# Performance work log

Measured on AMD Instinct MI355X. Metric: run time of the kernel, lower is better.

## Reference

```python
import jax, jax.numpy as jnp
import numpy as np
from jax import lax

B, N, C = 4, 4096, 512
HEADS, SR = 8, 4
HW = 64  # spatial size, HW*HW == N
EPS = 1e-5


def setup_inputs() -> dict:
    key = jax.random.key(0)
    ks = jax.random.split(key, 12)
    s = 0.02
    return {
        "x": jax.random.normal(ks[0], (B, N, C), jnp.float32),
        "wq": jax.random.normal(ks[1], (C, C), jnp.float32) * s,
        "bq": jnp.zeros((C,), jnp.float32),
        "wk": jax.random.normal(ks[2], (C, C), jnp.float32) * s,
        "bk": jnp.zeros((C,), jnp.float32),
        "wv": jax.random.normal(ks[3], (C, C), jnp.float32) * s,
        "bv": jnp.zeros((C,), jnp.float32),
        "w_sr": jax.random.normal(ks[4], (SR, SR, C, C), jnp.float32) * s,  # HWIO
        "b_sr": jnp.zeros((C,), jnp.float32),
        "gamma": jnp.ones((C,), jnp.float32),
        "beta": jnp.zeros((C,), jnp.float32),
        "wp": jax.random.normal(ks[5], (C, C), jnp.float32) * s,
        "bp": jnp.zeros((C,), jnp.float32),
    }


def _layernorm(x, gamma, beta):
    mu = jnp.mean(x, axis=-1, keepdims=True)
    var = jnp.mean(jnp.square(x - mu), axis=-1, keepdims=True)
    return (x - mu) * lax.rsqrt(var + EPS) * gamma + beta


def reference(x, wq, bq, wk, bk, wv, bv, w_sr, b_sr, gamma, beta, wp, bp):
    b, n, c = x.shape
    dh = c // HEADS
    scale = dh ** (-0.5)
    # Q at full resolution: [b, heads, n, dh]
    q = (x @ wq + bq).reshape(b, n, HEADS, dh).transpose(0, 2, 1, 3)
    # spatial reduction of K/V: conv stride=kernel=SR (VALID)
    xr = x.reshape(b, HW, HW, c)
    xr = lax.conv_general_dilated(
        xr, w_sr, window_strides=(SR, SR), padding="VALID",
        dimension_numbers=("NHWC", "HWIO", "NHWC")) + b_sr
    xr = xr.reshape(b, -1, c)  # [b, n_kv, c]
    xr = _layernorm(xr, gamma, beta)
    n_kv = xr.shape[1]
    k = (xr @ wk + bk).reshape(b, n_kv, HEADS, dh).transpose(0, 2, 1, 3)
    v = (xr @ wv + bv).reshape(b, n_kv, HEADS, dh).transpose(0, 2, 1, 3)
    attn = jnp.einsum("bhqd,bhkd->bhqk", q, k) * scale
    attn = jax.nn.softmax(attn, axis=-1)
    out = jnp.einsum("bhqk,bhkd->bhqd", attn, v)
    out = out.transpose(0, 2, 1, 3).reshape(b, n, c)
    return out @ wp + bp
```

## Files before the change

### kernel.cpp

```cpp
#include <hip/hip_runtime.h>
#include <hip/hip_bf16.h>


#define EPSV 1e-5f
#define SCALE_Q 0.18033688011112042f

typedef __attribute__((ext_vector_type(8))) short short8v;
typedef __attribute__((ext_vector_type(4))) short short4v;
typedef __attribute__((ext_vector_type(4))) float float4v;

static __device__ __forceinline__ ushort f2bf_bits(float x) {
  __hip_bfloat16 h = __float2bfloat16(x);
  return *(ushort*)&h;
}

static __device__ __forceinline__ float4v mfma16(short8v a, short8v b, float4v c) {
  return __builtin_amdgcn_mfma_f32_16x16x32_bf16(a, b, c, 0, 0, 0);
}

static __device__ __forceinline__ void wr_chunk(ushort* lds, int base, int4 v) {
  *(int2*)&lds[base]       = make_int2(v.x, v.y);
  *(int2*)&lds[base + 128] = make_int2(v.z, v.w);
}

static __device__ __forceinline__ void tile_t32(const float* __restrict__ src, int srcld,
                                                ushort* __restrict__ dst, int dstld,
                                                int kr0, int c0, int tid, float (*t)[33]) {
  {
    const int r = tid >> 3, c4 = (tid & 7) * 4;
    const float4 v = *(const float4*)&src[(size_t)(kr0 + r) * srcld + c0 + c4];
    t[r][c4 + 0] = v.x; t[r][c4 + 1] = v.y; t[r][c4 + 2] = v.z; t[r][c4 + 3] = v.w;
  }
  __syncthreads();
  {
    const int n = tid >> 3, k4 = (tid & 7) * 4;
    short4v o;
#pragma unroll
    for (int i = 0; i < 4; ++i) o[i] = (short)f2bf_bits(t[k4 + i][n]);
    *(short4v*)&dst[(size_t)(c0 + n) * dstld + kr0 + k4] = o;
  }
}

__global__ __launch_bounds__(256)
void prep(const float* __restrict__ x, const float* __restrict__ wq,
          const float* __restrict__ wk, const float* __restrict__ wv,
          const float* __restrict__ wp, const float* __restrict__ wsr,
          const float* __restrict__ bk, const float* __restrict__ bv,
          ushort* __restrict__ xbf, ushort* __restrict__ wqT,
          ushort* __restrict__ wkvT, ushort* __restrict__ wpT,
          ushort* __restrict__ wsrT, float* __restrict__ bkv) {
  __shared__ float t[32][33];
  const int bid = blockIdx.x, tid = threadIdx.x;
  if (bid < 4096) {
    const int i = bid * 256 + tid;
    const float4* s4 = (const float4*)x;
    const float4 a = s4[2 * i], b = s4[2 * i + 1];
    short8v v;
    v[0] = (short)f2bf_bits(a.x); v[1] = (short)f2bf_bits(a.y);
    v[2] = (short)f2bf_bits(a.z); v[3] = (short)f2bf_bits(a.w);
    v[4] = (short)f2bf_bits(b.x); v[5] = (short)f2bf_bits(b.y);
    v[6] = (short)f2bf_bits(b.z); v[7] = (short)f2bf_bits(b.w);
    *(short8v*)&xbf[(size_t)i * 8] = v;
  } else if (bid < 8192) {
    const int tI = bid - 4096;
    const int kr0 = (tI & 255) * 32, c0 = (tI >> 8) * 32;
    tile_t32(wsr, 512, wsrT, 8192, kr0, c0, tid, t);
  } else if (bid < 9216) {
    const int wsel = (bid - 8192) >> 8;
    const int tI = (bid - 8192) & 255;
    const int kr0 = (tI & 15) * 32, c0 = (tI >> 4) * 32;
    const float* src = wsel == 0 ? wq : wsel == 1 ? wk : wsel == 2 ? wv : wp;
    ushort* dst = wsel == 0 ? wqT : wsel == 1 ? wkvT : wsel == 2 ? (wkvT + 262144) : wpT;
    tile_t32(src, 512, dst, 512, kr0, c0, tid, t);
  } else {
    const int i4 = tid * 4;
    const float4 v = (i4 < 512) ? *(const float4*)&bk[i4] : *(const float4*)&bv[i4 - 512];
    *(float4*)&bkv[i4] = v;
  }
}

template<int MODE>
__global__ __launch_bounds__(256)
void gemm_bf(const ushort* __restrict__ A, const ushort* __restrict__ BT,
             const float* __restrict__ bias, void* __restrict__ outp,
             int M, int N, int K, float scale) {
  __shared__ ushort lds[8192];
  const int tid = threadIdx.x;
  const int wave = tid >> 6, lane = tid & 63;
  const int wm = wave >> 1, wn = wave & 1;
  const int bm = blockIdx.x * 128, bn = blockIdx.y * 128;
  const int lid = lane & 15, lg = lane >> 4;
  const int r0 = tid >> 2, c8 = tid & 3;
  const int g0 = 2 * (c8 & 1), h2 = c8 >> 1;
  const int c0 = c8 * 8;
  const int basew = ((r0 >> 4) * 64 + 16 * g0 + (r0 & 15)) * 8 + h2 * 4;
  float4v acc[4][4];
  const float4v zf = {0.f, 0.f, 0.f, 0.f};
#pragma unroll
  for (int mi = 0; mi < 4; ++mi)
#pragma unroll
    for (int ni = 0; ni < 4; ++ni) acc[mi][ni] = zf;
  const ushort* Ar0 = A + (size_t)(bm + r0) * K;
  const ushort* Ar1 = Ar0 + (size_t)64 * K;
  const ushort* Br0 = BT + (size_t)(bn + r0) * K;
  const ushort* Br1 = Br0 + (size_t)64 * K;
  const int NK = K >> 5;
  int koff = c0;
  int4 pa0 = *(const int4*)(Ar0 + koff), pa1 = *(const int4*)(Ar1 + koff);
  int4 pb0 = *(const int4*)(Br0 + koff), pb1 = *(const int4*)(Br1 + koff);
  for (int kb = 0; kb < NK; ++kb) {
    wr_chunk(lds, basew, pa0);
    wr_chunk(lds, basew + 2048, pa1);
    wr_chunk(lds, basew + 4096, pb0);
    wr_chunk(lds, basew + 6144, pb1);
    __syncthreads();
    if (kb + 1 < NK) {
      koff += 32;
      pa0 = *(const int4*)(Ar0 + koff); pa1 = *(const int4*)(Ar1 + koff);
      pb0 = *(const int4*)(Br0 + koff); pb1 = *(const int4*)(Br1 + koff);
    }
    short8v af[4], bfr[4];
#pragma unroll
    for (int mi = 0; mi < 4; ++mi)
      af[mi] = *(const short8v*)&lds[((wm * 4 + mi) * 64 + lane) * 8];
#pragma unroll
    for (int ni = 0; ni < 4; ++ni)
      bfr[ni] = *(const short8v*)&lds[4096 + ((wn * 4 + ni) * 64 + lane) * 8];
#pragma unroll
    for (int mi = 0; mi < 4; ++mi)
#pragma unroll
      for (int ni = 0; ni < 4; ++ni) acc[mi][ni] = mfma16(af[mi], bfr[ni], acc[mi][ni]);
    __syncthreads();
  }
  float bvv[4];
#pragma unroll
  for (int ni = 0; ni < 4; ++ni) bvv[ni] = bias[bn + wn * 64 + ni * 16 + lid];
#pragma unroll
  for (int mi = 0; mi < 4; ++mi)
#pragma unroll
    for (int ni = 0; ni < 4; ++ni) {
      const int col = bn + wn * 64 + ni * 16 + lid;
#pragma unroll
      for (int reg = 0; reg < 4; ++reg) {
        const int row = bm + wm * 64 + mi * 16 + 4 * lg + reg;
        const float v = (acc[mi][ni][reg] + bvv[ni]) * scale;
        if (MODE == 0) ((float*)outp)[(size_t)row * N + col] = v;
        else if (MODE == 1) ((ushort*)outp)[(size_t)row * N + col] = f2bf_bits(v);
        else {
          if (col < 512) ((ushort*)outp)[(size_t)row * 512 + col] = f2bf_bits(v);
          else ((ushort*)outp)[524288 + (size_t)(col - 512) * 1024 + row] = f2bf_bits(v);
        }
      }
    }
}

static __device__ __forceinline__ int4 ld_patch(const ushort* xbf, int b, int oh, int ow, int kg) {
  const int ij = kg >> 9, ci = kg & 511;
  const int n = (oh * 4 + (ij >> 2)) * 64 + ow * 4 + (ij & 3);
  return *(const int4*)(xbf + ((size_t)b * 4096 + n) * 512 + ci);
}

__global__ __launch_bounds__(256)
void conv_bf(const ushort* __restrict__ xbf, const ushort* __restrict__ wsrT,
             float* __restrict__ part) {
  __shared__ ushort lds[8192];
  const int tid = threadIdx.x;
  const int wave = tid >> 6, lane = tid & 63;
  const int wm = wave >> 1, wn = wave & 1;
  const int bm = blockIdx.x * 128, bn = blockIdx.y * 128, z = blockIdx.z;
  const int lid = lane & 15, lg = lane >> 4;
  const int r0 = tid >> 2, c8 = tid & 3;
  const int g0 = 2 * (c8 & 1), h2 = c8 >> 1;
  const int c0 = c8 * 8;
  const int basew = ((r0 >> 4) * 64 + 16 * g0 + (r0 & 15)) * 8 + h2 * 4;
  const int p0 = bm + r0, p1 = p0 + 64;
  const int b0 = p0 >> 8, oh0 = (p0 & 255) >> 4, ow0 = p0 & 15;
  const int b1 = p1 >> 8, oh1 = (p1 & 255) >> 4, ow1 = p1 & 15;
  const ushort* Br0 = wsrT + (size_t)(bn + r0) * 8192;
  const ushort* Br1 = Br0 + (size_t)64 * 8192;
  float4v acc[4][4];
  const float4v zf = {0.f, 0.f, 0.f, 0.f};
#pragma unroll
  for (int mi = 0; mi < 4; ++mi)
#pragma unroll
    for (int ni = 0; ni < 4; ++ni) acc[mi][ni] = zf;
  int kg = z * 512 + c0;
  int4 pa0 = ld_patch(xbf, b0, oh0, ow0, kg);
  int4 pa1 = ld_patch(xbf, b1, oh1, ow1, kg);
  int4 pb0 = *(const int4*)(Br0 + kg);
  int4 pb1 = *(const int4*)(Br1 + kg);
  for (int kb = 0; kb < 16; ++kb) {
    wr_chunk(lds, basew, pa0);
    wr_chunk(lds, basew + 2048, pa1);
    wr_chunk(lds, basew + 4096, pb0);
    wr_chunk(lds, basew + 6144, pb1);
    __syncthreads();
    if (kb < 15) {
      kg += 32;
      pa0 = ld_patch(xbf, b0, oh0, ow0, kg);
      pa1 = ld_patch(xbf, b1, oh1, ow1, kg);
      pb0 = *(const int4*)(Br0 + kg);
      pb1 = *(const int4*)(Br1 + kg);
    }
    short8v af[4], bfr[4];
#pragma unroll
    for (int mi = 0; mi < 4; ++mi)
      af[mi] = *(const short8v*)&lds[((wm * 4 + mi) * 64 + lane) * 8];
#pragma unroll
    for (int ni = 0; ni < 4; ++ni)
      bfr[ni] = *(const short8v*)&lds[4096 + ((wn * 4 + ni) * 64 + lane) * 8];
#pragma unroll
    for (int mi = 0; mi < 4; ++mi)
#pragma unroll
      for (int ni = 0; ni < 4; ++ni) acc[mi][ni] = mfma16(af[mi], bfr[ni], acc[mi][ni]);
    __syncthreads();
  }
#pragma unroll
  for (int mi = 0; mi < 4; ++mi)
#pragma unroll
    for (int ni = 0; ni < 4; ++ni)
#pragma unroll
      for (int reg = 0; reg < 4; ++reg)
        part[(size_t)(z * 1024 + bm + wm * 64 + mi * 16 + 4 * lg + reg) * 512 +
             bn + wn * 64 + ni * 16 + lid] = acc[mi][ni][reg];
}

__global__ __launch_bounds__(256)
void reduce_ln(const float* __restrict__ part, const float* __restrict__ bsr,
               const float* __restrict__ gamma, const float* __restrict__ beta,
               ushort* __restrict__ xln) {
  const int wave = threadIdx.x >> 6;
  const int lane = threadIdx.x & 63;
  const int row = blockIdx.x * 4 + wave;
  const int c = lane * 8;
  float v[8];
  {
    const float4 a = *(const float4*)&bsr[c];
    const float4 b = *(const float4*)&bsr[c + 4];
    v[0] = a.x; v[1] = a.y; v[2] = a.z; v[3] = a.w;
    v[4] = b.x; v[5] = b.y; v[6] = b.z; v[7] = b.w;
  }
#pragma unroll
  for (int z = 0; z < 16; ++z) {
    const float* pr = &part[((size_t)z * 1024 + row) * 512 + c];
    const float4 a = *(const float4*)pr;
    const float4 b = *(const float4*)(pr + 4);
    v[0] += a.x; v[1] += a.y; v[2] += a.z; v[3] += a.w;
    v[4] += b.x; v[5] += b.y; v[6] += b.z; v[7] += b.w;
  }
  float sum = 0.f;
#pragma unroll
  for (int i = 0; i < 8; ++i) sum += v[i];
#pragma unroll
  for (int off = 32; off >= 1; off >>= 1) sum += __shfl_xor(sum, off);
  const float mu = sum * (1.0f / 512.0f);
  float sq = 0.f;
#pragma unroll
  for (int i = 0; i < 8; ++i) { v[i] -= mu; sq += v[i] * v[i]; }
#pragma unroll
  for (int off = 32; off >= 1; off >>= 1) sq += __shfl_xor(sq, off);
  const float rs = rsqrtf(sq * (1.0f / 512.0f) + EPSV);
  const float4 g1 = *(const float4*)&gamma[c];
  const float4 g2 = *(const float4*)&gamma[c + 4];
  const float4 e1 = *(const float4*)&beta[c];
  const float4 e2 = *(const float4*)&beta[c + 4];
  const float g[8] = {g1.x, g1.y, g1.z, g1.w, g2.x, g2.y, g2.z, g2.w};
  const float e[8] = {e1.x, e1.y, e1.z, e1.w, e2.x, e2.y, e2.z, e2.w};
  short8v ov;
#pragma unroll
  for (int i = 0; i < 8; ++i) ov[i] = (short)f2bf_bits(v[i] * rs * g[i] + e[i]);
  *(short8v*)&xln[(size_t)row * 512 + c] = ov;
}

__global__ __launch_bounds__(256)
void attn_bf(const ushort* __restrict__ qbf, const ushort* __restrict__ kbf,
             const ushort* __restrict__ vt, ushort* __restrict__ attno) {
  __shared__ ushort kv_lds[16384];
  const int bh = blockIdx.x, qt = blockIdx.y;
  const int b = bh >> 3, h = bh & 7;
  const int tid = threadIdx.x;
  const int wave = tid >> 6, lane = tid & 63;
  const int lid = lane & 15, lg = lane >> 4;
  {
    const ushort* Kb = kbf + (size_t)(b * 256) * 512 + h * 64;
#pragma unroll
    for (int i = 0; i < 8; ++i) {
      const int u = i * 256 + tid;
      const int kv = u >> 3, c8 = u & 7, d0 = c8 * 8;
      const int4 d = *(const int4*)(Kb + (size_t)kv * 512 + d0);
      const int f = (kv >> 4) * 2 + (d0 >> 5);
      const int g0 = (d0 >> 2) & 3, hh2 = (d0 >> 4) & 1;
      wr_chunk(kv_lds, (f * 64 + 16 * g0 + (kv & 15)) * 8 + hh2 * 4, d);
    }
  }
  short8v qfr[2][2];
  const int qrow0 = qt * 128 + wave * 32;
#pragma unroll
  for (int qf = 0; qf < 2; ++qf)
#pragma unroll
    for (int t = 0; t < 2; ++t) {
      const size_t base = (size_t)(b * 4096 + qrow0 + qf * 16 + lid) * 512 + h * 64 + 32 * t + 4 * lg;
      const short4v lo = *(const short4v*)&qbf[base];
      const short4v hi = *(const short4v*)&qbf[base + 16];
      short8v q;
      q[0] = lo[0]; q[1] = lo[1]; q[2] = lo[2]; q[3] = lo[3];
      q[4] = hi[0]; q[5] = hi[1]; q[6] = hi[2]; q[7] = hi[3];
      qfr[qf][t] = q;
    }
  __syncthreads();
  float4v s[16][2];
  const float4v zf = {0.f, 0.f, 0.f, 0.f};
#pragma unroll
  for (int kvf = 0; kvf < 16; ++kvf) { s[kvf][0] = zf; s[kvf][1] = zf; }
#pragma unroll
  for (int kvf = 0; kvf < 16; ++kvf)
#pragma unroll
    for (int t = 0; t < 2; ++t) {
      const short8v ka = *(const short8v*)&kv_lds[((kvf * 2 + t) * 64 + lane) * 8];
      s[kvf][0] = mfma16(ka, qfr[0][t], s[kvf][0]);
      s[kvf][1] = mfma16(ka, qfr[1][t], s[kvf][1]);
    }
  float inv[2];
#pragma unroll
  for (int qf = 0; qf < 2; ++qf) {
    float m = -1e30f;
#pragma unroll
    for (int kvf = 0; kvf < 16; ++kvf)
#pragma unroll
      for (int e = 0; e < 4; ++e) m = fmaxf(m, s[kvf][qf][e]);
    m = fmaxf(m, __shfl_xor(m, 16));
    m = fmaxf(m, __shfl_xor(m, 32));
    float sum = 0.f;
#pragma unroll
    for (int kvf = 0; kvf < 16; ++kvf)
#pragma unroll
      for (int e = 0; e < 4; ++e) {
        const float p = __builtin_amdgcn_exp2f(s[kvf][qf][e] - m);
        s[kvf][qf][e] = p;
        sum += p;
      }
    sum += __shfl_xor(sum, 16);
    sum += __shfl_xor(sum, 32);
    inv[qf] = 1.0f / sum;
  }
  __syncthreads();
  {
    const ushort* Vb = vt + (size_t)(h * 64) * 1024 + b * 256;
#pragma unroll
    for (int i = 0; i < 8; ++i) {
      const int u = i * 256 + tid;
      const int d = u >> 5, c8 = u & 31, kv0 = c8 * 8;
      const int4 dd = *(const int4*)(Vb + (size_t)d * 1024 + kv0);
      const int f = (d >> 4) * 8 + (kv0 >> 5);
      const int g0 = (kv0 >> 2) & 3, hh2 = (kv0 >> 4) & 1;
      wr_chunk(kv_lds, (f * 64 + 16 * g0 + (d & 15)) * 8 + hh2 * 4, dd);
    }
  }
  __syncthreads();
  float4v o[2][4];
#pragma unroll
  for (int qf = 0; qf < 2; ++qf)
#pragma unroll
    for (int nf = 0; nf < 4; ++nf) o[qf][nf] = zf;
#pragma unroll
  for (int t = 0; t < 8; ++t) {
    short8v vb[4];
#pragma unroll
    for (int nf = 0; nf < 4; ++nf)
      vb[nf] = *(const short8v*)&kv_lds[((nf * 8 + t) * 64 + lane) * 8];
#pragma unroll
    for (int qf = 0; qf < 2; ++qf) {
      short8v pa;
#pragma unroll
      for (int j = 0; j < 4; ++j) {
        pa[j]     = (short)f2bf_bits(s[2 * t][qf][j]);
        pa[4 + j] = (short)f2bf_bits(s[2 * t + 1][qf][j]);
      }
#pragma unroll
      for (int nf = 0; nf < 4; ++nf) o[qf][nf] = mfma16(pa, vb[nf], o[qf][nf]);
    }
  }
#pragma unroll
  for (int qf = 0; qf < 2; ++qf) {
    float sc[4];
#pragma unroll
    for (int reg = 0; reg < 4; ++reg) sc[reg] = __shfl(inv[qf], 4 * lg + reg);
#pragma unroll
    for (int nf = 0; nf < 4; ++nf)
#pragma unroll
      for (int reg = 0; reg < 4; ++reg) {
        const int q = qrow0 + qf * 16 + 4 * lg + reg;
        const int c = h * 64 + nf * 16 + lid;
        attno[(size_t)(b * 4096 + q) * 512 + c] = f2bf_bits(o[qf][nf][reg] * sc[reg]);
      }
  }
}

extern "C" void kernel_launch(void* const* d_in, const int* in_sizes, int n_in,
                              void* d_out, int out_size, void* d_ws, size_t ws_size,
                              hipStream_t stream) {
  const float* x     = (const float*)d_in[0];
  const float* wq    = (const float*)d_in[1];
  const float* bq    = (const float*)d_in[2];
  const float* wk    = (const float*)d_in[3];
  const float* bk    = (const float*)d_in[4];
  const float* wv    = (const float*)d_in[5];
  const float* bv    = (const float*)d_in[6];
  const float* wsr   = (const float*)d_in[7];
  const float* bsr   = (const float*)d_in[8];
  const float* gamma = (const float*)d_in[9];
  const float* beta  = (const float*)d_in[10];
  const float* wp    = (const float*)d_in[11];
  const float* bp    = (const float*)d_in[12];
  float* out = (float*)d_out;

  char* w = (char*)d_ws;
  ushort* xbf   = (ushort*)(w);
  ushort* qbf   = (ushort*)(w + 16777216);
  ushort* attno = (ushort*)(w + 33554432);
  float*  part  = (float*) (w + 50331648);
  ushort* wsrT  = (ushort*)(w + 83886080);
  ushort* wqT   = (ushort*)(w + 92274688);
  ushort* wpT   = (ushort*)(w + 92798976);
  ushort* wkvT  = (ushort*)(w + 93323264);
  ushort* xln   = (ushort*)(w + 94371840);
  ushort* kbf   = (ushort*)(w + 95420416);
  ushort* vt    = (ushort*)(w + 96468992);
  float*  bkv   = (float*) (w + 97517568);

  prep<<<9217, 256, 0, stream>>>(x, wq, wk, wv, wp, wsr, bk, bv,
                                 xbf, wqT, wkvT, wpT, wsrT, bkv);
  conv_bf<<<dim3(8, 4, 16), 256, 0, stream>>>(xbf, wsrT, part);
  reduce_ln<<<256, 256, 0, stream>>>(part, bsr, gamma, beta, xln);
  gemm_bf<2><<<dim3(8, 8), 256, 0, stream>>>(xln, wkvT, bkv, kbf, 1024, 1024, 512, 1.0f);
  gemm_bf<1><<<dim3(128, 4), 256, 0, stream>>>(xbf, wqT, bq, qbf, 16384, 512, 512, SCALE_Q);
  attn_bf<<<dim3(32, 32), 256, 0, stream>>>(qbf, kbf, vt, attno);
  gemm_bf<0><<<dim3(128, 4), 256, 0, stream>>>(attno, wpT, bp, out, 16384, 512, 512, 1.0f);
}
```

Before: 217.4 us.

## Fuse Q projection into attention kernel and pre-swizzle K/V into LDS image layout

The separate Q-projection GEMM is removed. Each attention block now computes its 128x64 Q tile directly from bf16 x and the transposed wq with MFMA, which avoids writing and re-reading the 16 MB qbf buffer and saves a launch. The KV GEMM epilogue writes K and V straight into the per-(batch,head) swizzled LDS layout, so the attention kernel loads them with plain contiguous int4 copies, and the V load is issued early to overlap with softmax. The cost is a redundant Q recomputation per head block (K=512 loop), more LDS per block, and scattered 2-byte stores in the KV GEMM epilogue.

Result: slower. 236.8 us (+8.9%).

```diff
diff --git a/kernel.cpp b/kernel.cpp
--- a/kernel.cpp
+++ b/kernel.cpp
@@ -144,11 +144,25 @@
       for (int reg = 0; reg < 4; ++reg) {
         const int row = bm + wm * 64 + mi * 16 + 4 * lg + reg;
         const float v = (acc[mi][ni][reg] + bvv[ni]) * scale;
-        if (MODE == 0) ((float*)outp)[(size_t)row * N + col] = v;
-        else if (MODE == 1) ((ushort*)outp)[(size_t)row * N + col] = f2bf_bits(v);
-        else {
-          if (col < 512) ((ushort*)outp)[(size_t)row * 512 + col] = f2bf_bits(v);
-          else ((ushort*)outp)[524288 + (size_t)(col - 512) * 1024 + row] = f2bf_bits(v);
+        if (MODE == 0) {
+          ((float*)outp)[(size_t)row * N + col] = v;
+        } else {
+          ushort* img = (ushort*)outp;
+          const int bb = row >> 8, kv = row & 255;
+          if (col < 512) {
+            const int hh = col >> 6, d = col & 63;
+            img[(size_t)(bb * 8 + hh) * 16384 +
+                ((kv >> 4) * 2 + (d >> 5)) * 512 +
+                ((kv & 15) + (((d >> 2) & 3) << 4)) * 8 +
+                (d & 3) + (((d >> 4) & 1) << 2)] = f2bf_bits(v);
+          } else {
+            const int c2 = col - 512;
+            const int hh = c2 >> 6, d = c2 & 63;
+            (img + 524288)[(size_t)(bb * 8 + hh) * 16384 +
+                ((d >> 4) * 8 + (kv >> 5)) * 512 +
+                ((d & 15) + (((kv >> 2) & 3) << 4)) * 8 +
+                (kv & 3) + (((kv >> 4) & 1) << 2)] = f2bf_bits(v);
+          }
         }
       }
     }
@@ -273,43 +287,77 @@
 }
 
 __global__ __launch_bounds__(256)
-void attn_bf(const ushort* __restrict__ qbf, const ushort* __restrict__ kbf,
-             const ushort* __restrict__ vt, ushort* __restrict__ attno) {
-  __shared__ ushort kv_lds[16384];
+void attn_fused(const ushort* __restrict__ xbf, const ushort* __restrict__ wqT,
+                const float* __restrict__ bq, const ushort* __restrict__ kvimg,
+                ushort* __restrict__ attno) {
+  __shared__ ushort kv_lds[22528];
   const int bh = blockIdx.x, qt = blockIdx.y;
   const int b = bh >> 3, h = bh & 7;
   const int tid = threadIdx.x;
   const int wave = tid >> 6, lane = tid & 63;
   const int lid = lane & 15, lg = lane >> 4;
-  {
-    const ushort* Kb = kbf + (size_t)(b * 256) * 512 + h * 64;
-#pragma unroll
-    for (int i = 0; i < 8; ++i) {
-      const int u = i * 256 + tid;
-      const int kv = u >> 3, c8 = u & 7, d0 = c8 * 8;
-      const int4 d = *(const int4*)(Kb + (size_t)kv * 512 + d0);
-      const int f = (kv >> 4) * 2 + (d0 >> 5);
-      const int g0 = (d0 >> 2) & 3, hh2 = (d0 >> 4) & 1;
-      wr_chunk(kv_lds, (f * 64 + 16 * g0 + (kv & 15)) * 8 + hh2 * 4, d);
-    }
+  const ushort* kimg = kvimg + (size_t)bh * 16384;
+  const ushort* vimg = kvimg + 524288 + (size_t)bh * 16384;
+  int4 kreg[8];
+#pragma unroll
+  for (int c = 0; c < 8; ++c)
+    kreg[c] = *(const int4*)(kimg + (c * 256 + tid) * 8);
+  const int r0 = tid >> 2, c8 = tid & 3;
+  const int g0 = 2 * (c8 & 1), h2 = c8 >> 1;
+  const int basew = ((r0 >> 4) * 64 + 16 * g0 + (r0 & 15)) * 8 + h2 * 4;
+  ushort* qs = kv_lds + 16384;
+  const ushort* Xr0 = xbf + (size_t)(b * 4096 + qt * 128 + r0) * 512;
+  const ushort* Xr1 = Xr0 + (size_t)64 * 512;
+  const ushort* Wr  = wqT + (size_t)(h * 64 + r0) * 512;
+  float4v accq[4][2];
+  const float4v zf = {0.f, 0.f, 0.f, 0.f};
+#pragma unroll
+  for (int dd = 0; dd < 4; ++dd) { accq[dd][0] = zf; accq[dd][1] = zf; }
+  int koff = c8 * 8;
+  int4 px0 = *(const int4*)(Xr0 + koff);
+  int4 px1 = *(const int4*)(Xr1 + koff);
+  int4 pw  = *(const int4*)(Wr + koff);
+  for (int kt = 0; kt < 16; ++kt) {
+    wr_chunk(qs, basew, px0);
+    wr_chunk(qs, basew + 2048, px1);
+    wr_chunk(qs, basew + 4096, pw);
+    __syncthreads();
+    if (kt < 15) {
+      koff += 32;
+      px0 = *(const int4*)(Xr0 + koff);
+      px1 = *(const int4*)(Xr1 + koff);
+      pw  = *(const int4*)(Wr + koff);
+    }
+    const short8v xf0 = *(const short8v*)&qs[((wave * 2 + 0) * 64 + lane) * 8];
+    const short8v xf1 = *(const short8v*)&qs[((wave * 2 + 1) * 64 + lane) * 8];
+#pragma unroll
+    for (int dd = 0; dd < 4; ++dd) {
+      const short8v wf = *(const short8v*)&qs[4096 + (dd * 64 + lane) * 8];
+      accq[dd][0] = mfma16(wf, xf0, accq[dd][0]);
+      accq[dd][1] = mfma16(wf, xf1, accq[dd][1]);
+    }
+    __syncthreads();
   }
   short8v qfr[2][2];
-  const int qrow0 = qt * 128 + wave * 32;
-#pragma unroll
-  for (int qf = 0; qf < 2; ++qf)
-#pragma unroll
-    for (int t = 0; t < 2; ++t) {
-      const size_t base = (size_t)(b * 4096 + qrow0 + qf * 16 + lid) * 512 + h * 64 + 32 * t + 4 * lg;
-      const short4v lo = *(const short4v*)&qbf[base];
-      const short4v hi = *(const short4v*)&qbf[base + 16];
-      short8v q;
-      q[0] = lo[0]; q[1] = lo[1]; q[2] = lo[2]; q[3] = lo[3];
-      q[4] = hi[0]; q[5] = hi[1]; q[6] = hi[2]; q[7] = hi[3];
-      qfr[qf][t] = q;
-    }
+#pragma unroll
+  for (int t = 0; t < 2; ++t)
+#pragma unroll
+    for (int odd = 0; odd < 2; ++odd) {
+      const int dd = 2 * t + odd;
+      const float4 b4 = *(const float4*)&bq[h * 64 + dd * 16 + 4 * lg];
+      const float bb[4] = {b4.x, b4.y, b4.z, b4.w};
+#pragma unroll
+      for (int qf = 0; qf < 2; ++qf)
+#pragma unroll
+        for (int reg = 0; reg < 4; ++reg)
+          qfr[qf][t][reg + 4 * odd] =
+              (short)f2bf_bits((accq[dd][qf][reg] + bb[reg]) * SCALE_Q);
+    }
+#pragma unroll
+  for (int c = 0; c < 8; ++c)
+    *(int4*)&kv_lds[(c * 256 + tid) * 8] = kreg[c];
   __syncthreads();
   float4v s[16][2];
-  const float4v zf = {0.f, 0.f, 0.f, 0.f};
 #pragma unroll
   for (int kvf = 0; kvf < 16; ++kvf) { s[kvf][0] = zf; s[kvf][1] = zf; }
 #pragma unroll
@@ -320,6 +368,14 @@
       s[kvf][0] = mfma16(ka, qfr[0][t], s[kvf][0]);
       s[kvf][1] = mfma16(ka, qfr[1][t], s[kvf][1]);
     }
+  int4 vreg[8];
+#pragma unroll
+  for (int c = 0; c < 8; ++c)
+    vreg[c] = *(const int4*)(vimg + (c * 256 + tid) * 8);
+  __syncthreads();
+#pragma unroll
+  for (int c = 0; c < 8; ++c)
+    *(int4*)&kv_lds[(c * 256 + tid) * 8] = vreg[c];
   float inv[2];
 #pragma unroll
   for (int qf = 0; qf < 2; ++qf) {
@@ -344,19 +400,6 @@
     inv[qf] = 1.0f / sum;
   }
   __syncthreads();
-  {
-    const ushort* Vb = vt + (size_t)(h * 64) * 1024 + b * 256;
-#pragma unroll
-    for (int i = 0; i < 8; ++i) {
-      const int u = i * 256 + tid;
-      const int d = u >> 5, c8 = u & 31, kv0 = c8 * 8;
-      const int4 dd = *(const int4*)(Vb + (size_t)d * 1024 + kv0);
-      const int f = (d >> 4) * 8 + (kv0 >> 5);
-      const int g0 = (kv0 >> 2) & 3, hh2 = (kv0 >> 4) & 1;
-      wr_chunk(kv_lds, (f * 64 + 16 * g0 + (d & 15)) * 8 + hh2 * 4, dd);
-    }
-  }
-  __syncthreads();
   float4v o[2][4];
 #pragma unroll
   for (int qf = 0; qf < 2; ++qf)
@@ -380,6 +423,7 @@
       for (int nf = 0; nf < 4; ++nf) o[qf][nf] = mfma16(pa, vb[nf], o[qf][nf]);
     }
   }
+  const int qrow0 = qt * 128 + wave * 32;
 #pragma unroll
   for (int qf = 0; qf < 2; ++qf) {
     float sc[4];
@@ -416,24 +460,21 @@
 
   char* w = (char*)d_ws;
   ushort* xbf   = (ushort*)(w);
-  ushort* qbf   = (ushort*)(w + 16777216);
-  ushort* attno = (ushort*)(w + 33554432);
-  float*  part  = (float*) (w + 50331648);
-  ushort* wsrT  = (ushort*)(w + 83886080);
-  ushort* wqT   = (ushort*)(w + 92274688);
-  ushort* wpT   = (ushort*)(w + 92798976);
-  ushort* wkvT  = (ushort*)(w + 93323264);
-  ushort* xln   = (ushort*)(w + 94371840);
-  ushort* kbf   = (ushort*)(w + 95420416);
-  ushort* vt    = (ushort*)(w + 96468992);
-  float*  bkv   = (float*) (w + 97517568);
+  ushort* attno = (ushort*)(w + 16777216);
+  float*  part  = (float*) (w + 33554432);
+  ushort* wsrT  = (ushort*)(w + 67108864);
+  ushort* wqT   = (ushort*)(w + 75497472);
+  ushort* wpT   = (ushort*)(w + 76021760);
+  ushort* wkvT  = (ushort*)(w + 76546048);
+  ushort* xln   = (ushort*)(w + 77594624);
+  ushort* kvimg = (ushort*)(w + 78643200);
+  float*  bkv   = (float*) (w + 80740352);
 
   prep<<<9217, 256, 0, stream>>>(x, wq, wk, wv, wp, wsr, bk, bv,
                                  xbf, wqT, wkvT, wpT, wsrT, bkv);
   conv_bf<<<dim3(8, 4, 16), 256, 0, stream>>>(xbf, wsrT, part);
   reduce_ln<<<256, 256, 0, stream>>>(part, bsr, gamma, beta, xln);
-  gemm_bf<2><<<dim3(8, 8), 256, 0, stream>>>(xln, wkvT, bkv, kbf, 1024, 1024, 512, 1.0f);
-  gemm_bf<1><<<dim3(128, 4), 256, 0, stream>>>(xbf, wqT, bq, qbf, 16384, 512, 512, SCALE_Q);
-  attn_bf<<<dim3(32, 32), 256, 0, stream>>>(qbf, kbf, vt, attno);
+  gemm_bf<2><<<dim3(8, 8), 256, 0, stream>>>(xln, wkvT, bkv, kvimg, 1024, 1024, 512, 1.0f);
+  attn_fused<<<dim3(32, 32), 256, 0, stream>>>(xbf, wqT, bq, kvimg, attno);
   gemm_bf<0><<<dim3(128, 4), 256, 0, stream>>>(attno, wpT, bp, out, 16384, 512, 512, 1.0f);
 }
```

## Store operands in MFMA-fragment image layout and drop LDS staging in GEMMs/attention

Applied to the files above, without the earlier changes.

Producers (prep, reduce_ln, GEMM epilogues, attention output) now write activations and weights directly in a pre-swizzled per-lane MFMA fragment layout. The GEMMs and the attention kernel then load fragments straight from global memory with one 16-byte load per lane, removing LDS staging, the shuffle writes and the barriers. The cost is that every tile read now goes to global memory or cache rather than shared LDS, so data reuse across waves depends on L2. Producer epilogues also gain scattered stores.

Result: slower. 231.8 us (+6.6%).

```diff
diff --git a/kernel.cpp b/kernel.cpp
--- a/kernel.cpp
+++ b/kernel.cpp
@@ -18,27 +18,15 @@
   return __builtin_amdgcn_mfma_f32_16x16x32_bf16(a, b, c, 0, 0, 0);
 }
 
+static __device__ __forceinline__ size_t img_idx(int row, int k, int KC) {
+  const int rt = row >> 7, kc = k >> 5, f = (row >> 4) & 7, lid = row & 15;
+  const int k32 = k & 31, lg = (k32 >> 2) & 3, j = (k32 & 3) + ((k32 >> 4) & 1) * 4;
+  return ((size_t)(rt * KC + kc) * 8 + f) * 512 + (lid + 16 * lg) * 8 + j;
+}
+
 static __device__ __forceinline__ void wr_chunk(ushort* lds, int base, int4 v) {
   *(int2*)&lds[base]       = make_int2(v.x, v.y);
   *(int2*)&lds[base + 128] = make_int2(v.z, v.w);
-}
-
-static __device__ __forceinline__ void tile_t32(const float* __restrict__ src, int srcld,
-                                                ushort* __restrict__ dst, int dstld,
-                                                int kr0, int c0, int tid, float (*t)[33]) {
-  {
-    const int r = tid >> 3, c4 = (tid & 7) * 4;
-    const float4 v = *(const float4*)&src[(size_t)(kr0 + r) * srcld + c0 + c4];
-    t[r][c4 + 0] = v.x; t[r][c4 + 1] = v.y; t[r][c4 + 2] = v.z; t[r][c4 + 3] = v.w;
-  }
-  __syncthreads();
-  {
-    const int n = tid >> 3, k4 = (tid & 7) * 4;
-    short4v o;
-#pragma unroll
-    for (int i = 0; i < 4; ++i) o[i] = (short)f2bf_bits(t[k4 + i][n]);
-    *(short4v*)&dst[(size_t)(c0 + n) * dstld + kr0 + k4] = o;
-  }
 }
 
 __global__ __launch_bounds__(256)
@@ -46,9 +34,10 @@
           const float* __restrict__ wk, const float* __restrict__ wv,
           const float* __restrict__ wp, const float* __restrict__ wsr,
           const float* __restrict__ bk, const float* __restrict__ bv,
-          ushort* __restrict__ xbf, ushort* __restrict__ wqT,
-          ushort* __restrict__ wkvT, ushort* __restrict__ wpT,
-          ushort* __restrict__ wsrT, float* __restrict__ bkv) {
+          ushort* __restrict__ xbf, ushort* __restrict__ ximg,
+          ushort* __restrict__ wqimg, ushort* __restrict__ wkvimg,
+          ushort* __restrict__ wpimg, ushort* __restrict__ wsrT,
+          float* __restrict__ bkv) {
   __shared__ float t[32][33];
   const int bid = blockIdx.x, tid = threadIdx.x;
   if (bid < 4096) {
@@ -61,97 +50,55 @@
     v[4] = (short)f2bf_bits(b.x); v[5] = (short)f2bf_bits(b.y);
     v[6] = (short)f2bf_bits(b.z); v[7] = (short)f2bf_bits(b.w);
     *(short8v*)&xbf[(size_t)i * 8] = v;
+    const int row = i >> 6, c = (i & 63) * 8;
+    const int rt = row >> 7, f = (row >> 4) & 7, lid = row & 15;
+    const int kc = c >> 5, k32 = c & 31, lg0 = (k32 >> 2) & 3, j0 = ((k32 >> 4) & 1) * 4;
+    ushort* basep = ximg + ((size_t)(rt * 16 + kc) * 8 + f) * 512 + j0;
+    const int4 vi = *(const int4*)&v;
+    *(int2*)&basep[(lid + 16 * lg0) * 8] = make_int2(vi.x, vi.y);
+    *(int2*)&basep[(lid + 16 * (lg0 + 1)) * 8] = make_int2(vi.z, vi.w);
   } else if (bid < 8192) {
     const int tI = bid - 4096;
     const int kr0 = (tI & 255) * 32, c0 = (tI >> 8) * 32;
-    tile_t32(wsr, 512, wsrT, 8192, kr0, c0, tid, t);
+    {
+      const int r = tid >> 3, c4 = (tid & 7) * 4;
+      const float4 v = *(const float4*)&wsr[(size_t)(kr0 + r) * 512 + c0 + c4];
+      t[r][c4 + 0] = v.x; t[r][c4 + 1] = v.y; t[r][c4 + 2] = v.z; t[r][c4 + 3] = v.w;
+    }
+    __syncthreads();
+    {
+      const int n = tid >> 3, k4 = (tid & 7) * 4;
+      short4v o;
+#pragma unroll
+      for (int i = 0; i < 4; ++i) o[i] = (short)f2bf_bits(t[k4 + i][n]);
+      *(short4v*)&wsrT[(size_t)(c0 + n) * 8192 + kr0 + k4] = o;
+    }
   } else if (bid < 9216) {
     const int wsel = (bid - 8192) >> 8;
     const int tI = (bid - 8192) & 255;
     const int kr0 = (tI & 15) * 32, c0 = (tI >> 4) * 32;
     const float* src = wsel == 0 ? wq : wsel == 1 ? wk : wsel == 2 ? wv : wp;
-    ushort* dst = wsel == 0 ? wqT : wsel == 1 ? wkvT : wsel == 2 ? (wkvT + 262144) : wpT;
-    tile_t32(src, 512, dst, 512, kr0, c0, tid, t);
+    ushort* dst = wsel == 0 ? wqimg : wsel == 3 ? wpimg : wkvimg;
+    const int colbase = (wsel == 2) ? 512 : 0;
+    {
+      const int r = tid >> 3, c4 = (tid & 7) * 4;
+      const float4 v = *(const float4*)&src[(size_t)(kr0 + r) * 512 + c0 + c4];
+      t[r][c4 + 0] = v.x; t[r][c4 + 1] = v.y; t[r][c4 + 2] = v.z; t[r][c4 + 3] = v.w;
+    }
+    __syncthreads();
+    {
+      const int n = tid >> 3, k4 = (tid & 7) * 4;
+      const int col = colbase + c0 + n, k = kr0 + k4;
+      short4v o;
+#pragma unroll
+      for (int i = 0; i < 4; ++i) o[i] = (short)f2bf_bits(t[k4 + i][n]);
+      *(short4v*)&dst[img_idx(col, k, 16)] = o;
+    }
   } else {
     const int i4 = tid * 4;
     const float4 v = (i4 < 512) ? *(const float4*)&bk[i4] : *(const float4*)&bv[i4 - 512];
     *(float4*)&bkv[i4] = v;
   }
-}
-
-template<int MODE>
-__global__ __launch_bounds__(256)
-void gemm_bf(const ushort* __restrict__ A, const ushort* __restrict__ BT,
-             const float* __restrict__ bias, void* __restrict__ outp,
-             int M, int N, int K, float scale) {
-  __shared__ ushort lds[8192];
-  const int tid = threadIdx.x;
-  const int wave = tid >> 6, lane = tid & 63;
-  const int wm = wave >> 1, wn = wave & 1;
-  const int bm = blockIdx.x * 128, bn = blockIdx.y * 128;
-  const int lid = lane & 15, lg = lane >> 4;
-  const int r0 = tid >> 2, c8 = tid & 3;
-  const int g0 = 2 * (c8 & 1), h2 = c8 >> 1;
-  const int c0 = c8 * 8;
-  const int basew = ((r0 >> 4) * 64 + 16 * g0 + (r0 & 15)) * 8 + h2 * 4;
-  float4v acc[4][4];
-  const float4v zf = {0.f, 0.f, 0.f, 0.f};
-#pragma unroll
-  for (int mi = 0; mi < 4; ++mi)
-#pragma unroll
-    for (int ni = 0; ni < 4; ++ni) acc[mi][ni] = zf;
-  const ushort* Ar0 = A + (size_t)(bm + r0) * K;
-  const ushort* Ar1 = Ar0 + (size_t)64 * K;
-  const ushort* Br0 = BT + (size_t)(bn + r0) * K;
-  const ushort* Br1 = Br0 + (size_t)64 * K;
-  const int NK = K >> 5;
-  int koff = c0;
-  int4 pa0 = *(const int4*)(Ar0 + koff), pa1 = *(const int4*)(Ar1 + koff);
-  int4 pb0 = *(const int4*)(Br0 + koff), pb1 = *(const int4*)(Br1 + koff);
-  for (int kb = 0; kb < NK; ++kb) {
-    wr_chunk(lds, basew, pa0);
-    wr_chunk(lds, basew + 2048, pa1);
-    wr_chunk(lds, basew + 4096, pb0);
-    wr_chunk(lds, basew + 6144, pb1);
-    __syncthreads();
-    if (kb + 1 < NK) {
-      koff += 32;
-      pa0 = *(const int4*)(Ar0 + koff); pa1 = *(const int4*)(Ar1 + koff);
-      pb0 = *(const int4*)(Br0 + koff); pb1 = *(const int4*)(Br1 + koff);
-    }
-    short8v af[4], bfr[4];
-#pragma unroll
-    for (int mi = 0; mi < 4; ++mi)
-      af[mi] = *(const short8v*)&lds[((wm * 4 + mi) * 64 + lane) * 8];
-#pragma unroll
-    for (int ni = 0; ni < 4; ++ni)
-      bfr[ni] = *(const short8v*)&lds[4096 + ((wn * 4 + ni) * 64 + lane) * 8];
-#pragma unroll
-    for (int mi = 0; mi < 4; ++mi)
-#pragma unroll
-      for (int ni = 0; ni < 4; ++ni) acc[mi][ni] = mfma16(af[mi], bfr[ni], acc[mi][ni]);
-    __syncthreads();
-  }
-  float bvv[4];
-#pragma unroll
-  for (int ni = 0; ni < 4; ++ni) bvv[ni] = bias[bn + wn * 64 + ni * 16 + lid];
-#pragma unroll
-  for (int mi = 0; mi < 4; ++mi)
-#pragma unroll
-    for (int ni = 0; ni < 4; ++ni) {
-      const int col = bn + wn * 64 + ni * 16 + lid;
-#pragma unroll
-      for (int reg = 0; reg < 4; ++reg) {
-        const int row = bm + wm * 64 + mi * 16 + 4 * lg + reg;
-        const float v = (acc[mi][ni][reg] + bvv[ni]) * scale;
-        if (MODE == 0) ((float*)outp)[(size_t)row * N + col] = v;
-        else if (MODE == 1) ((ushort*)outp)[(size_t)row * N + col] = f2bf_bits(v);
-        else {
-          if (col < 512) ((ushort*)outp)[(size_t)row * 512 + col] = f2bf_bits(v);
-          else ((ushort*)outp)[524288 + (size_t)(col - 512) * 1024 + row] = f2bf_bits(v);
-        }
-      }
-    }
 }
 
 static __device__ __forceinline__ int4 ld_patch(const ushort* xbf, int b, int oh, int ow, int kg) {
@@ -228,7 +175,7 @@
 __global__ __launch_bounds__(256)
 void reduce_ln(const float* __restrict__ part, const float* __restrict__ bsr,
                const float* __restrict__ gamma, const float* __restrict__ beta,
-               ushort* __restrict__ xln) {
+               ushort* __restrict__ xlnimg) {
   const int wave = threadIdx.x >> 6;
   const int lane = threadIdx.x & 63;
   const int row = blockIdx.x * 4 + wave;
@@ -269,45 +216,108 @@
   short8v ov;
 #pragma unroll
   for (int i = 0; i < 8; ++i) ov[i] = (short)f2bf_bits(v[i] * rs * g[i] + e[i]);
-  *(short8v*)&xln[(size_t)row * 512 + c] = ov;
-}
-
+  const int rt = row >> 7, f = (row >> 4) & 7, lid = row & 15;
+  const int kc = c >> 5, k32 = c & 31, lg0 = (k32 >> 2) & 3, j0 = ((k32 >> 4) & 1) * 4;
+  ushort* basep = xlnimg + ((size_t)(rt * 16 + kc) * 8 + f) * 512 + j0;
+  const int4 vi = *(const int4*)&ov;
+  *(int2*)&basep[(lid + 16 * lg0) * 8] = make_int2(vi.x, vi.y);
+  *(int2*)&basep[(lid + 16 * (lg0 + 1)) * 8] = make_int2(vi.z, vi.w);
+}
+
+template<int MODE>
 __global__ __launch_bounds__(256)
-void attn_bf(const ushort* __restrict__ qbf, const ushort* __restrict__ kbf,
-             const ushort* __restrict__ vt, ushort* __restrict__ attno) {
-  __shared__ ushort kv_lds[16384];
+void gemm_img(const ushort* __restrict__ Aimg, const ushort* __restrict__ Bimg,
+              const float* __restrict__ bias, void* __restrict__ outp, float scale) {
+  constexpr int KC = 16;
+  const int tid = threadIdx.x;
+  const int wave = tid >> 6, lane = tid & 63;
+  const int wm = wave >> 1, wn = wave & 1;
+  const int rt = blockIdx.x, ct = blockIdx.y;
+  const int lid = lane & 15, lg = lane >> 4;
+  const ushort* Ab = Aimg + ((size_t)rt * KC * 8 + wm * 4) * 512 + lane * 8;
+  const ushort* Bb = Bimg + ((size_t)ct * KC * 8 + wn * 4) * 512 + lane * 8;
+  float4v acc[4][4];
+  const float4v zf = {0.f, 0.f, 0.f, 0.f};
+#pragma unroll
+  for (int mi = 0; mi < 4; ++mi)
+#pragma unroll
+    for (int ni = 0; ni < 4; ++ni) acc[mi][ni] = zf;
+#pragma unroll
+  for (int kb = 0; kb < KC; ++kb) {
+    short8v af[4], bf[4];
+#pragma unroll
+    for (int mi = 0; mi < 4; ++mi)
+      af[mi] = *(const short8v*)(Ab + (size_t)kb * 4096 + mi * 512);
+#pragma unroll
+    for (int ni = 0; ni < 4; ++ni)
+      bf[ni] = *(const short8v*)(Bb + (size_t)kb * 4096 + ni * 512);
+#pragma unroll
+    for (int mi = 0; mi < 4; ++mi)
+#pragma unroll
+      for (int ni = 0; ni < 4; ++ni) acc[mi][ni] = mfma16(af[mi], bf[ni], acc[mi][ni]);
+  }
+  float bvv[4];
+#pragma unroll
+  for (int ni = 0; ni < 4; ++ni) bvv[ni] = bias[ct * 128 + wn * 64 + ni * 16 + lid];
+#pragma unroll
+  for (int mi = 0; mi < 4; ++mi)
+#pragma unroll
+    for (int ni = 0; ni < 4; ++ni) {
+      const int col = ct * 128 + wn * 64 + ni * 16 + lid;
+#pragma unroll
+      for (int reg = 0; reg < 4; ++reg) {
+        const int row = rt * 128 + wm * 64 + mi * 16 + 4 * lg + reg;
+        const float v = (acc[mi][ni][reg] + bvv[ni]) * scale;
+        if (MODE == 0) {
+          ((float*)outp)[(size_t)row * 512 + col] = v;
+        } else if (MODE == 2) {
+          ushort* img = (ushort*)outp;
+          const int bb = row >> 8, kv = row & 255;
+          if (col < 512) {
+            const int hh = col >> 6, d = col & 63;
+            img[(size_t)(bb * 8 + hh) * 16384 +
+                ((kv >> 4) * 2 + (d >> 5)) * 512 +
+                ((kv & 15) + (((d >> 2) & 3) << 4)) * 8 +
+                (d & 3) + (((d >> 4) & 1) << 2)] = f2bf_bits(v);
+          } else {
+            const int c2 = col - 512;
+            const int hh = c2 >> 6, d = c2 & 63;
+            (img + 524288)[(size_t)(bb * 8 + hh) * 16384 +
+                ((d >> 4) * 8 + (kv >> 5)) * 512 +
+                ((d & 15) + (((kv >> 2) & 3) << 4)) * 8 +
+                (kv & 3) + (((kv >> 4) & 1) << 2)] = f2bf_bits(v);
+          }
+        } else {
+          ushort* img = (ushort*)outp;
+          const int bq_ = row >> 12, n = row & 4095;
+          const int qtt = n >> 7, nn = n & 127;
+          const int wv_ = nn >> 5, qf = (nn >> 4) & 1, lidq = nn & 15;
+          const int h = col >> 6, d = col & 63, tt = d >> 5, d32 = d & 31;
+          const int lgq = (d32 >> 2) & 3, jq = (d32 & 3) + ((d32 >> 4) & 1) * 4;
+          img[((size_t)(((bq_ * 8 + h) * 32 + qtt) * 4 + wv_) * 4 + qf * 2 + tt) * 512 +
+              (lidq + 16 * lgq) * 8 + jq] = f2bf_bits(v);
+        }
+      }
+    }
+}
+
+__global__ __launch_bounds__(256)
+void attn_img(const ushort* __restrict__ qimg, const ushort* __restrict__ kvimg,
+              ushort* __restrict__ oimg) {
   const int bh = blockIdx.x, qt = blockIdx.y;
   const int b = bh >> 3, h = bh & 7;
   const int tid = threadIdx.x;
   const int wave = tid >> 6, lane = tid & 63;
   const int lid = lane & 15, lg = lane >> 4;
-  {
-    const ushort* Kb = kbf + (size_t)(b * 256) * 512 + h * 64;
-#pragma unroll
-    for (int i = 0; i < 8; ++i) {
-      const int u = i * 256 + tid;
-      const int kv = u >> 3, c8 = u & 7, d0 = c8 * 8;
-      const int4 d = *(const int4*)(Kb + (size_t)kv * 512 + d0);
-      const int f = (kv >> 4) * 2 + (d0 >> 5);
-      const int g0 = (d0 >> 2) & 3, hh2 = (d0 >> 4) & 1;
-      wr_chunk(kv_lds, (f * 64 + 16 * g0 + (kv & 15)) * 8 + hh2 * 4, d);
-    }
-  }
+  const ushort* kb_ = kvimg + (size_t)bh * 16384;
+  const ushort* vb_ = kvimg + 524288 + (size_t)bh * 16384;
+  const ushort* qb_ = qimg + ((size_t)((bh * 32 + qt) * 4 + wave) * 4) * 512 + lane * 8;
   short8v qfr[2][2];
-  const int qrow0 = qt * 128 + wave * 32;
 #pragma unroll
   for (int qf = 0; qf < 2; ++qf)
 #pragma unroll
-    for (int t = 0; t < 2; ++t) {
-      const size_t base = (size_t)(b * 4096 + qrow0 + qf * 16 + lid) * 512 + h * 64 + 32 * t + 4 * lg;
-      const short4v lo = *(const short4v*)&qbf[base];
-      const short4v hi = *(const short4v*)&qbf[base + 16];
-      short8v q;
-      q[0] = lo[0]; q[1] = lo[1]; q[2] = lo[2]; q[3] = lo[3];
-      q[4] = hi[0]; q[5] = hi[1]; q[6] = hi[2]; q[7] = hi[3];
-      qfr[qf][t] = q;
-    }
-  __syncthreads();
+    for (int t = 0; t < 2; ++t)
+      qfr[qf][t] = *(const short8v*)(qb_ + (qf * 2 + t) * 512);
   float4v s[16][2];
   const float4v zf = {0.f, 0.f, 0.f, 0.f};
 #pragma unroll
@@ -316,7 +326,7 @@
   for (int kvf = 0; kvf < 16; ++kvf)
 #pragma unroll
     for (int t = 0; t < 2; ++t) {
-      const short8v ka = *(const short8v*)&kv_lds[((kvf * 2 + t) * 64 + lane) * 8];
+      const short8v ka = *(const short8v*)(kb_ + ((kvf * 2 + t) * 64 + lane) * 8);
       s[kvf][0] = mfma16(ka, qfr[0][t], s[kvf][0]);
       s[kvf][1] = mfma16(ka, qfr[1][t], s[kvf][1]);
     }
@@ -343,20 +353,6 @@
     sum += __shfl_xor(sum, 32);
     inv[qf] = 1.0f / sum;
   }
-  __syncthreads();
-  {
-    const ushort* Vb = vt + (size_t)(h * 64) * 1024 + b * 256;
-#pragma unroll
-    for (int i = 0; i < 8; ++i) {
-      const int u = i * 256 + tid;
-      const int d = u >> 5, c8 = u & 31, kv0 = c8 * 8;
-      const int4 dd = *(const int4*)(Vb + (size_t)d * 1024 + kv0);
-      const int f = (d >> 4) * 8 + (kv0 >> 5);
-      const int g0 = (kv0 >> 2) & 3, hh2 = (kv0 >> 4) & 1;
-      wr_chunk(kv_lds, (f * 64 + 16 * g0 + (d & 15)) * 8 + hh2 * 4, dd);
-    }
-  }
-  __syncthreads();
   float4v o[2][4];
 #pragma unroll
   for (int qf = 0; qf < 2; ++qf)
@@ -367,7 +363,7 @@
     short8v vb[4];
 #pragma unroll
     for (int nf = 0; nf < 4; ++nf)
-      vb[nf] = *(const short8v*)&kv_lds[((nf * 8 + t) * 64 + lane) * 8];
+      vb[nf] = *(const short8v*)(vb_ + ((nf * 8 + t) * 64 + lane) * 8);
 #pragma unroll
     for (int qf = 0; qf < 2; ++qf) {
       short8v pa;
@@ -380,19 +376,23 @@
       for (int nf = 0; nf < 4; ++nf) o[qf][nf] = mfma16(pa, vb[nf], o[qf][nf]);
     }
   }
+  const int rt_o = b * 32 + qt;
 #pragma unroll
   for (int qf = 0; qf < 2; ++qf) {
     float sc[4];
 #pragma unroll
     for (int reg = 0; reg < 4; ++reg) sc[reg] = __shfl(inv[qf], 4 * lg + reg);
-#pragma unroll
-    for (int nf = 0; nf < 4; ++nf)
-#pragma unroll
-      for (int reg = 0; reg < 4; ++reg) {
-        const int q = qrow0 + qf * 16 + 4 * lg + reg;
-        const int c = h * 64 + nf * 16 + lid;
-        attno[(size_t)(b * 4096 + q) * 512 + c] = f2bf_bits(o[qf][nf][reg] * sc[reg]);
-      }
+    const int f_o = wave * 2 + qf;
+#pragma unroll
+    for (int nf = 0; nf < 4; ++nf) {
+      const int colc = h * 64 + nf * 16 + lid;
+      const int kc = colc >> 5, k32 = colc & 31;
+      const int lgk = (k32 >> 2) & 3, jk = (k32 & 3) + ((k32 >> 4) & 1) * 4;
+      ushort* basep = oimg + ((size_t)(rt_o * 16 + kc) * 8 + f_o) * 512 + 16 * lgk * 8 + jk;
+#pragma unroll
+      for (int reg = 0; reg < 4; ++reg)
+        basep[(4 * lg + reg) * 8] = f2bf_bits(o[qf][nf][reg] * sc[reg]);
+    }
   }
 }
 
@@ -415,25 +415,25 @@
   float* out = (float*)d_out;
 
   char* w = (char*)d_ws;
-  ushort* xbf   = (ushort*)(w);
-  ushort* qbf   = (ushort*)(w + 16777216);
-  ushort* attno = (ushort*)(w + 33554432);
-  float*  part  = (float*) (w + 50331648);
-  ushort* wsrT  = (ushort*)(w + 83886080);
-  ushort* wqT   = (ushort*)(w + 92274688);
-  ushort* wpT   = (ushort*)(w + 92798976);
-  ushort* wkvT  = (ushort*)(w + 93323264);
-  ushort* xln   = (ushort*)(w + 94371840);
-  ushort* kbf   = (ushort*)(w + 95420416);
-  ushort* vt    = (ushort*)(w + 96468992);
-  float*  bkv   = (float*) (w + 97517568);
+  ushort* xbf    = (ushort*)(w);
+  ushort* ximg   = (ushort*)(w + 16777216);
+  float*  part   = (float*) (w + 33554432);
+  ushort* qimg   = (ushort*)(w + 33554432);
+  ushort* oimg   = (ushort*)(w + 50331648);
+  ushort* wsrT   = (ushort*)(w + 67108864);
+  ushort* wqimg  = (ushort*)(w + 75497472);
+  ushort* wpimg  = (ushort*)(w + 76021760);
+  ushort* wkvimg = (ushort*)(w + 76546048);
+  ushort* xlnimg = (ushort*)(w + 77594624);
+  ushort* kvimg  = (ushort*)(w + 78643200);
+  float*  bkv    = (float*) (w + 80740352);
 
   prep<<<9217, 256, 0, stream>>>(x, wq, wk, wv, wp, wsr, bk, bv,
-                                 xbf, wqT, wkvT, wpT, wsrT, bkv);
+                                 xbf, ximg, wqimg, wkvimg, wpimg, wsrT, bkv);
   conv_bf<<<dim3(8, 4, 16), 256, 0, stream>>>(xbf, wsrT, part);
-  reduce_ln<<<256, 256, 0, stream>>>(part, bsr, gamma, beta, xln);
-  gemm_bf<2><<<dim3(8, 8), 256, 0, stream>>>(xln, wkvT, bkv, kbf, 1024, 1024, 512, 1.0f);
-  gemm_bf<1><<<dim3(128, 4), 256, 0, stream>>>(xbf, wqT, bq, qbf, 16384, 512, 512, SCALE_Q);
-  attn_bf<<<dim3(32, 32), 256, 0, stream>>>(qbf, kbf, vt, attno);
-  gemm_bf<0><<<dim3(128, 4), 256, 0, stream>>>(attno, wpT, bp, out, 16384, 512, 512, 1.0f);
-}
+  reduce_ln<<<256, 256, 0, stream>>>(part, bsr, gamma, beta, xlnimg);
+  gemm_img<2><<<dim3(8, 8), 256, 0, stream>>>(xlnimg, wkvimg, bkv, kvimg, 1.0f);
+  gemm_img<3><<<dim3(128, 4), 256, 0, stream>>>(ximg, wqimg, bq, qimg, SCALE_Q);
+  attn_img<<<dim3(32, 32), 256, 0, stream>>>(qimg, kvimg, oimg);
+  gemm_img<0><<<dim3(128, 4), 256, 0, stream>>>(oimg, wpimg, bp, out, 1.0f);
+}
```
